# Optimization experiments

Measured on AMD Instinct MI355X. Metric: run time of the kernel, lower is better.

## Reference

```python
import jax, jax.numpy as jnp
import numpy as np

HEADS = 16
HEAD_DIM = 64  # embed_size // heads = 1024 // 16


def setup_inputs() -> dict:
    key = jax.random.key(0)
    ks = jax.random.split(key, 9)
    N, Sq, E, C = 4, 2048, 1024, 512
    Skv = 2 * Sq  # keys/values seq must equal doubled query seq (see view trick)
    return {
        "values": jax.random.normal(ks[0], (N, Skv, E), dtype=jnp.float32),
        "keys": jax.random.normal(ks[1], (N, Skv, E), dtype=jnp.float32),
        "queries": jax.random.normal(ks[2], (N, Sq, E), dtype=jnp.float32),
        "mask": jax.random.randint(ks[3], (N, Skv, HEADS, HEADS), 0, 2, dtype=jnp.int32),
        "condition": jax.random.normal(ks[4], (N, Sq, C), dtype=jnp.float32),
        "Wc": jax.random.normal(ks[5], (E, C), dtype=jnp.float32) * 0.02,
        "bc": jax.random.normal(ks[6], (E,), dtype=jnp.float32) * 0.02,
        "Wo": jax.random.normal(ks[7], (E, E), dtype=jnp.float32) * 0.02,
        "bo": jax.random.normal(ks[8], (E,), dtype=jnp.float32) * 0.02,
    }


def reference(values, keys, queries, mask, condition, Wc, bc, Wo, bo):
    N = queries.shape[0]
    H, D = HEADS, HEAD_DIM
    # condition_linear + concat: (N, Sq, 2E) -> view doubles seq -> (N, 2Sq, H, D)
    cond_feat = jnp.einsum('nsc,ec->nse', condition, Wc) + bc
    cq = jnp.concatenate([queries, cond_feat], axis=-1).reshape(N, -1, H, D)
    k = keys.reshape(N, -1, H, D)    # (N, 2Sq, H, D)
    v = values.reshape(N, -1, H, D)  # (N, 2Sq, H, D)
    # per-(batch,seq) heads-by-heads attention, exactly as the torch matmul does
    att = jnp.einsum('nshd,nsed->nshe', cq, k) / jnp.sqrt(jnp.float32(D))
    att = jnp.where(mask == 0, jnp.float32(-1e20), att)
    att = jax.nn.softmax(att, axis=-1)
    out = jnp.einsum('nshe,nsed->nshd', att, v).reshape(N, -1, H * D)
    return jnp.einsum('nsk,ek->nse', out, Wo) + bo
```

## Files before the change

kernel.cpp:

```cpp
#include <hip/hip_runtime.h>
#include <hip/hip_bf16.h>
#include <type_traits>

#define NB   4
#define SQ   2048
#define SKV  4096
#define EMB  1024
#define CDIM 512
#define POS  4

typedef __attribute__((ext_vector_type(8))) short short8;
typedef __attribute__((ext_vector_type(4))) float f32x4;

__device__ __forceinline__ float b2f(ushort u) {
    union { unsigned int i; float f; } v;
    v.i = ((unsigned int)u) << 16;
    return v.f;
}
__device__ __forceinline__ ushort f2b(float f) {
    union { float f; unsigned int i; } v; v.f = f;
    unsigned int x = v.i;
    return (ushort)((x + 0x7fffu + ((x >> 16) & 1u)) >> 16);
}

__device__ __forceinline__ void glds16(const ushort* gp, ushort* lp) {
    __builtin_amdgcn_global_load_lds(
        (const __attribute__((address_space(1))) unsigned int*)gp,
        (__attribute__((address_space(3))) unsigned int*)lp,
        16, 0, 0);
}

__global__ __launch_bounds__(256)
void cvt_f32_bf16(const float* __restrict__ in, ushort* __restrict__ out, int n4)
{
    const int i = blockIdx.x * 256 + threadIdx.x;
    if (i < n4) {
        float4 v = ((const float4*)in)[i];
        ushort4 o;
        o.x = f2b(v.x); o.y = f2b(v.y); o.z = f2b(v.z); o.w = f2b(v.w);
        ((ushort4*)out)[i] = o;
    }
}

template <typename OT>
__global__ __launch_bounds__(256)
void gemm_bt_bias(const ushort* __restrict__ A, const ushort* __restrict__ B,
                  const float* __restrict__ bias, OT* __restrict__ C,
                  int M, int Nn, int K)
{
    __shared__ __attribute__((aligned(16))) ushort As[128 * 32];
    __shared__ __attribute__((aligned(16))) ushort Bs[128 * 32];

    const int tid  = threadIdx.x;
    const int wave = tid >> 6;
    const int lane = tid & 63;
    const int quad = lane >> 4;
    const int l16  = lane & 15;
    const int wr   = wave >> 1;
    const int wc   = wave & 1;

    int mTile, nTile;
    {
        const int gx = gridDim.x, gy = gridDim.y;
        const int flat = blockIdx.y * gx + blockIdx.x;
        if ((gx & 7) == 0 && gy == 8) {
            const int c = flat & 7, j = flat >> 3;
            mTile = c * (gx >> 3) + (j >> 3);
            nTile = j & 7;
        } else {
            mTile = blockIdx.x; nTile = blockIdx.y;
        }
    }
    const long mBase = (long)mTile * 128;
    const long nBase = (long)nTile * 128;

    const ushort* Ablk = A + mBase * K;
    const ushort* Bblk = B + nBase * K;

    const int lr = lane >> 2;
    const int lc = (lane & 3) * 8;
    const int c0 = wave * 2, c1 = wave * 2 + 1;
    const ushort* aG0 = Ablk + (long)(c0 * 16 + lr) * K + lc;
    const ushort* aG1 = Ablk + (long)(c1 * 16 + lr) * K + lc;
    const ushort* bG0 = Bblk + (long)(c0 * 16 + lr) * K + lc;
    const ushort* bG1 = Bblk + (long)(c1 * 16 + lr) * K + lc;
    ushort* aL0 = As + c0 * 512;
    ushort* aL1 = As + c1 * 512;
    ushort* bL0 = Bs + c0 * 512;
    ushort* bL1 = Bs + c1 * 512;

    f32x4 acc[4][4];
#pragma unroll
    for (int i = 0; i < 4; ++i)
#pragma unroll
        for (int j = 0; j < 4; ++j)
            acc[i][j] = (f32x4){0.f, 0.f, 0.f, 0.f};

    for (int k0 = 0; k0 < K; k0 += 32) {
        __syncthreads();
        glds16(aG0 + k0, aL0);
        glds16(aG1 + k0, aL1);
        glds16(bG0 + k0, bL0);
        glds16(bG1 + k0, bL1);
        __syncthreads();

        short8 af[4], bfr[4];
#pragma unroll
        for (int mt = 0; mt < 4; ++mt)
            af[mt] = *(const short8*)(As + (wr * 64 + mt * 16 + l16) * 32 + quad * 8);
#pragma unroll
        for (int nt = 0; nt < 4; ++nt)
            bfr[nt] = *(const short8*)(Bs + (wc * 64 + nt * 16 + l16) * 32 + quad * 8);

#pragma unroll
        for (int mt = 0; mt < 4; ++mt)
#pragma unroll
            for (int nt = 0; nt < 4; ++nt)
                acc[mt][nt] = __builtin_amdgcn_mfma_f32_16x16x32_bf16(
                    af[mt], bfr[nt], acc[mt][nt], 0, 0, 0);
    }

#pragma unroll
    for (int mt = 0; mt < 4; ++mt) {
#pragma unroll
        for (int nt = 0; nt < 4; ++nt) {
            const long n = nBase + wc * 64 + nt * 16 + l16;
            const float bv = bias[n];
#pragma unroll
            for (int r = 0; r < 4; ++r) {
                const long m = mBase + wr * 64 + mt * 16 + quad * 4 + r;
                if constexpr (std::is_same<OT, float>::value)
                    C[m * Nn + n] = acc[mt][nt][r] + bv;
                else
                    C[m * Nn + n] = f2b(acc[mt][nt][r] + bv);
            }
        }
    }
}

__global__ __launch_bounds__(256)
void attn_kernel(const float*  __restrict__ queries,
                 const ushort* __restrict__ condfeat,
                 const float*  __restrict__ keys,
                 const float*  __restrict__ values,
                 const int*    __restrict__ mask,
                 ushort* __restrict__ attout)
{
    const int tid     = threadIdx.x;
    const int basePos = blockIdx.x * POS;

    __shared__ __attribute__((aligned(16))) float cq[16 * 68];
    __shared__ __attribute__((aligned(16))) float ks[16 * 68];
    __shared__ __attribute__((aligned(16))) float vs[16 * 68];
    __shared__ float sc[16 * 17];

    const int base4 = tid * 4;
    const int hs = base4 >> 6, dsd = base4 & 63;

    auto loadQ = [&](int p) -> float4 {
        const int n = p >> 12, sh = (p & 4095) >> 1;
        float4 q4;
        if (p & 1) {
            const ushort* cp = condfeat + ((size_t)n * SQ + sh) * EMB + base4;
            ushort4 c4 = *(const ushort4*)cp;
            q4.x = b2f(c4.x); q4.y = b2f(c4.y); q4.z = b2f(c4.z); q4.w = b2f(c4.w);
        } else {
            q4 = *(const float4*)(queries + ((size_t)n * SQ + sh) * EMB + base4);
        }
        return q4;
    };

    float4 q4 = loadQ(basePos);
    float4 k4 = *(const float4*)(keys   + ((size_t)basePos << 10) + base4);
    float4 v4 = *(const float4*)(values + ((size_t)basePos << 10) + base4);
    int    mv = mask[((size_t)basePos << 8) + tid];

#pragma unroll
    for (int i = 0; i < POS; ++i) {
        const int p = basePos + i;

        *(float4*)(cq + hs * 68 + dsd) = q4;
        *(float4*)(ks + hs * 68 + dsd) = k4;
        *(float4*)(vs + hs * 68 + dsd) = v4;
        __syncthreads();

        float4 q4n, k4n, v4n; int mvn = 0;
        if (i + 1 < POS) {
            q4n = loadQ(p + 1);
            k4n = *(const float4*)(keys   + ((size_t)(p + 1) << 10) + base4);
            v4n = *(const float4*)(values + ((size_t)(p + 1) << 10) + base4);
            mvn = mask[((size_t)(p + 1) << 8) + tid];
        }

        {
            const int h = tid >> 4, e = tid & 15;
            float s = 0.f;
#pragma unroll
            for (int d = 0; d < 64; d += 4) {
                float4 a = *(const float4*)(cq + h * 68 + d);
                float4 b = *(const float4*)(ks + e * 68 + d);
                s += a.x * b.x + a.y * b.y + a.z * b.z + a.w * b.w;
            }
            s *= 0.125f;
            s = (mv == 0) ? -1e20f : s;

            float mx = s;
#pragma unroll
            for (int d = 1; d < 16; d <<= 1)
                mx = fmaxf(mx, __shfl_xor(mx, d));
            const float ex = __expf(s - mx);
            float sum = ex;
#pragma unroll
            for (int d = 1; d < 16; d <<= 1)
                sum += __shfl_xor(sum, d);
            sc[h * 17 + e] = ex / sum;
        }
        __syncthreads();

        {
            float4 a = {0.f, 0.f, 0.f, 0.f};
#pragma unroll
            for (int e = 0; e < 16; ++e) {
                const float pe = sc[hs * 17 + e];
                float4 vv = *(const float4*)(vs + e * 68 + dsd);
                a.x += pe * vv.x; a.y += pe * vv.y;
                a.z += pe * vv.z; a.w += pe * vv.w;
            }
            ushort4 o;
            o.x = f2b(a.x); o.y = f2b(a.y); o.z = f2b(a.z); o.w = f2b(a.w);
            *(ushort4*)(attout + ((size_t)p << 10) + base4) = o;
        }

        if (i + 1 < POS) {
            __syncthreads();
            q4 = q4n; k4 = k4n; v4 = v4n; mv = mvn;
        }
    }
}

extern "C" void kernel_launch(void* const* d_in, const int* in_sizes, int n_in,
                              void* d_out, int out_size, void* d_ws, size_t ws_size,
                              hipStream_t stream)
{
    const float* values    = (const float*)d_in[0];
    const float* keys      = (const float*)d_in[1];
    const float* queries   = (const float*)d_in[2];
    const int*   mask      = (const int*)  d_in[3];
    const float* condition = (const float*)d_in[4];
    const float* Wc        = (const float*)d_in[5];
    const float* bc        = (const float*)d_in[6];
    const float* Wo        = (const float*)d_in[7];
    const float* bo        = (const float*)d_in[8];
    float* out = (float*)d_out;

    ushort* condfeat = (ushort*)d_ws;
    ushort* attout   = condfeat + (size_t)NB * SQ * EMB;
    ushort* cond_bf  = attout;
    ushort* Wc_bf    = attout + (size_t)NB * SQ * CDIM;
    ushort* Wo_bf    = condfeat;

    cvt_f32_bf16<<<(NB * SQ * CDIM / 4 + 255) / 256, 256, 0, stream>>>(
        condition, cond_bf, NB * SQ * CDIM / 4);
    cvt_f32_bf16<<<(EMB * CDIM / 4 + 255) / 256, 256, 0, stream>>>(
        Wc, Wc_bf, EMB * CDIM / 4);

    {
        dim3 grid((NB * SQ) / 128, EMB / 128);
        gemm_bt_bias<ushort><<<grid, 256, 0, stream>>>(
            cond_bf, Wc_bf, bc, condfeat, NB * SQ, EMB, CDIM);
    }

    attn_kernel<<<(NB * SKV) / POS, 256, 0, stream>>>(queries, condfeat, keys,
                                                      values, mask, attout);

    cvt_f32_bf16<<<(EMB * EMB / 4 + 255) / 256, 256, 0, stream>>>(
        Wo, Wo_bf, EMB * EMB / 4);

    {
        dim3 grid((NB * SKV) / 128, EMB / 128);
        gemm_bt_bias<float><<<grid, 256, 0, stream>>>(
            attout, Wo_bf, bo, out, NB * SKV, EMB, EMB);
    }
}
```

Measured before the change: 311.8 us.

## Rewrite per-position attention with one wave per position using bf16 MFMA

The attention kernel now gives each wave its own sequence position instead of looping four positions through the whole block with block-wide barriers. The 16x16 head score matrix and the probability-times-V product are computed with bf16 MFMA instructions, with K and Q converted to bf16 in registers. V is staged into shared memory through asynchronous global-to-LDS loads, and softmax uses a few lane shuffles. This removes __syncthreads and scalar LDS dot products, but adds bf16 rounding of K, Q, V and the probabilities, plus lane-shuffle packing of the probability operand.

```diff
diff --git a/kernel.cpp b/kernel.cpp
--- a/kernel.cpp
+++ b/kernel.cpp
@@ -7,7 +7,6 @@
 #define SKV  4096
 #define EMB  1024
 #define CDIM 512
-#define POS  4
 
 typedef __attribute__((ext_vector_type(8))) short short8;
 typedef __attribute__((ext_vector_type(4))) float f32x4;
@@ -146,95 +145,108 @@
                  const int*    __restrict__ mask,
                  ushort* __restrict__ attout)
 {
-    const int tid     = threadIdx.x;
-    const int basePos = blockIdx.x * POS;
-
-    __shared__ __attribute__((aligned(16))) float cq[16 * 68];
-    __shared__ __attribute__((aligned(16))) float ks[16 * 68];
-    __shared__ __attribute__((aligned(16))) float vs[16 * 68];
-    __shared__ float sc[16 * 17];
-
-    const int base4 = tid * 4;
-    const int hs = base4 >> 6, dsd = base4 & 63;
-
-    auto loadQ = [&](int p) -> float4 {
-        const int n = p >> 12, sh = (p & 4095) >> 1;
-        float4 q4;
-        if (p & 1) {
-            const ushort* cp = condfeat + ((size_t)n * SQ + sh) * EMB + base4;
-            ushort4 c4 = *(const ushort4*)cp;
-            q4.x = b2f(c4.x); q4.y = b2f(c4.y); q4.z = b2f(c4.z); q4.w = b2f(c4.w);
-        } else {
-            q4 = *(const float4*)(queries + ((size_t)n * SQ + sh) * EMB + base4);
-        }
-        return q4;
-    };
-
-    float4 q4 = loadQ(basePos);
-    float4 k4 = *(const float4*)(keys   + ((size_t)basePos << 10) + base4);
-    float4 v4 = *(const float4*)(values + ((size_t)basePos << 10) + base4);
-    int    mv = mask[((size_t)basePos << 8) + tid];
-
-#pragma unroll
-    for (int i = 0; i < POS; ++i) {
-        const int p = basePos + i;
-
-        *(float4*)(cq + hs * 68 + dsd) = q4;
-        *(float4*)(ks + hs * 68 + dsd) = k4;
-        *(float4*)(vs + hs * 68 + dsd) = v4;
-        __syncthreads();
-
-        float4 q4n, k4n, v4n; int mvn = 0;
-        if (i + 1 < POS) {
-            q4n = loadQ(p + 1);
-            k4n = *(const float4*)(keys   + ((size_t)(p + 1) << 10) + base4);
-            v4n = *(const float4*)(values + ((size_t)(p + 1) << 10) + base4);
-            mvn = mask[((size_t)(p + 1) << 8) + tid];
-        }
-
-        {
-            const int h = tid >> 4, e = tid & 15;
-            float s = 0.f;
-#pragma unroll
-            for (int d = 0; d < 64; d += 4) {
-                float4 a = *(const float4*)(cq + h * 68 + d);
-                float4 b = *(const float4*)(ks + e * 68 + d);
-                s += a.x * b.x + a.y * b.y + a.z * b.z + a.w * b.w;
-            }
-            s *= 0.125f;
-            s = (mv == 0) ? -1e20f : s;
-
-            float mx = s;
-#pragma unroll
-            for (int d = 1; d < 16; d <<= 1)
-                mx = fmaxf(mx, __shfl_xor(mx, d));
-            const float ex = __expf(s - mx);
-            float sum = ex;
-#pragma unroll
-            for (int d = 1; d < 16; d <<= 1)
-                sum += __shfl_xor(sum, d);
-            sc[h * 17 + e] = ex / sum;
-        }
-        __syncthreads();
-
-        {
-            float4 a = {0.f, 0.f, 0.f, 0.f};
-#pragma unroll
-            for (int e = 0; e < 16; ++e) {
-                const float pe = sc[hs * 17 + e];
-                float4 vv = *(const float4*)(vs + e * 68 + dsd);
-                a.x += pe * vv.x; a.y += pe * vv.y;
-                a.z += pe * vv.z; a.w += pe * vv.w;
-            }
-            ushort4 o;
-            o.x = f2b(a.x); o.y = f2b(a.y); o.z = f2b(a.z); o.w = f2b(a.w);
-            *(ushort4*)(attout + ((size_t)p << 10) + base4) = o;
-        }
-
-        if (i + 1 < POS) {
-            __syncthreads();
-            q4 = q4n; k4 = k4n; v4 = v4n; mv = mvn;
-        }
+    __shared__ __attribute__((aligned(16))) float vbuf[4][1024];
+
+    const int tid  = threadIdx.x;
+    const int wave = tid >> 6;
+    const int lane = tid & 63;
+    const int l15  = lane & 15;
+    const int quad = lane >> 4;
+    const int p    = blockIdx.x * 4 + wave;
+    const int n    = p >> 12;
+    const int sh   = (p & 4095) >> 1;
+
+    float* vb = vbuf[wave];
+    const float* vrow = values + ((size_t)p << 10);
+#pragma unroll
+    for (int c = 0; c < 4; ++c)
+        glds16((const ushort*)(vrow + c * 256 + lane * 4),
+               (ushort*)(vb + c * 256));
+
+    const int4 mv = *(const int4*)(mask + ((size_t)p << 8) + l15 * 16 + quad * 4);
+
+    union SU { short8 v; ushort u[8]; uint w[4]; };
+
+    const float* krow = keys + ((size_t)p << 10);
+    SU ka, kb;
+    {
+        float kf[16];
+        *(float4*)&kf[0]  = *(const float4*)(krow + l15 * 64 + quad * 8);
+        *(float4*)&kf[4]  = *(const float4*)(krow + l15 * 64 + quad * 8 + 4);
+        *(float4*)&kf[8]  = *(const float4*)(krow + l15 * 64 + 32 + quad * 8);
+        *(float4*)&kf[12] = *(const float4*)(krow + l15 * 64 + 32 + quad * 8 + 4);
+#pragma unroll
+        for (int j = 0; j < 8; ++j) { ka.u[j] = f2b(kf[j]); kb.u[j] = f2b(kf[8 + j]); }
+    }
+
+    SU qa, qb;
+    if (p & 1) {
+        const ushort* crow = condfeat + (((size_t)n * SQ + sh) << 10);
+        qa.v = *(const short8*)(crow + l15 * 64 + quad * 8);
+        qb.v = *(const short8*)(crow + l15 * 64 + 32 + quad * 8);
+    } else {
+        const float* qrow = queries + (((size_t)n * SQ + sh) << 10);
+        float qf[16];
+        *(float4*)&qf[0]  = *(const float4*)(qrow + l15 * 64 + quad * 8);
+        *(float4*)&qf[4]  = *(const float4*)(qrow + l15 * 64 + quad * 8 + 4);
+        *(float4*)&qf[8]  = *(const float4*)(qrow + l15 * 64 + 32 + quad * 8);
+        *(float4*)&qf[12] = *(const float4*)(qrow + l15 * 64 + 32 + quad * 8 + 4);
+#pragma unroll
+        for (int j = 0; j < 8; ++j) { qa.u[j] = f2b(qf[j]); qb.u[j] = f2b(qf[8 + j]); }
+    }
+
+    f32x4 sacc = (f32x4){0.f, 0.f, 0.f, 0.f};
+    sacc = __builtin_amdgcn_mfma_f32_16x16x32_bf16(ka.v, qa.v, sacc, 0, 0, 0);
+    sacc = __builtin_amdgcn_mfma_f32_16x16x32_bf16(kb.v, qb.v, sacc, 0, 0, 0);
+
+    float s0 = (mv.x == 0) ? -1e20f : sacc[0] * 0.125f;
+    float s1 = (mv.y == 0) ? -1e20f : sacc[1] * 0.125f;
+    float s2 = (mv.z == 0) ? -1e20f : sacc[2] * 0.125f;
+    float s3 = (mv.w == 0) ? -1e20f : sacc[3] * 0.125f;
+
+    float mx = fmaxf(fmaxf(s0, s1), fmaxf(s2, s3));
+    mx = fmaxf(mx, __shfl_xor(mx, 16));
+    mx = fmaxf(mx, __shfl_xor(mx, 32));
+    const float e0 = __expf(s0 - mx), e1 = __expf(s1 - mx);
+    const float e2 = __expf(s2 - mx), e3 = __expf(s3 - mx);
+    float sum = e0 + e1 + e2 + e3;
+    sum += __shfl_xor(sum, 16);
+    sum += __shfl_xor(sum, 32);
+    const float inv = 1.f / sum;
+
+    const uint pk01 = (uint)f2b(e0 * inv) | ((uint)f2b(e1 * inv) << 16);
+    const uint pk23 = (uint)f2b(e2 * inv) | ((uint)f2b(e3 * inv) << 16);
+
+    const int srcA = (quad * 32 + l15) & 63;
+    const int srcB = (quad * 32 + 16 + l15) & 63;
+    SU pf;
+    {
+        const uint w0 = (uint)__shfl((int)pk01, srcA);
+        const uint w1 = (uint)__shfl((int)pk23, srcA);
+        const uint w2 = (uint)__shfl((int)pk01, srcB);
+        const uint w3 = (uint)__shfl((int)pk23, srcB);
+        const bool lo = (lane < 32);
+        pf.w[0] = lo ? w0 : 0u; pf.w[1] = lo ? w1 : 0u;
+        pf.w[2] = lo ? w2 : 0u; pf.w[3] = lo ? w3 : 0u;
+    }
+
+    asm volatile("s_waitcnt vmcnt(0)" ::: "memory");
+
+    ushort* orow = attout + ((size_t)p << 10);
+    const int eb = (quad & 1) * 8;
+#pragma unroll
+    for (int sl = 0; sl < 4; ++sl) {
+        const int d0 = sl * 16;
+        SU vf;
+#pragma unroll
+        for (int j = 0; j < 8; ++j)
+            vf.u[j] = f2b(vb[(eb + j) * 64 + d0 + l15]);
+        f32x4 oacc = (f32x4){0.f, 0.f, 0.f, 0.f};
+        oacc = __builtin_amdgcn_mfma_f32_16x16x32_bf16(vf.v, pf.v, oacc, 0, 0, 0);
+        ushort4 o;
+        o.x = f2b(oacc[0]); o.y = f2b(oacc[1]);
+        o.z = f2b(oacc[2]); o.w = f2b(oacc[3]);
+        *(ushort4*)(orow + l15 * 64 + d0 + quad * 4) = o;
     }
 }
 
@@ -270,8 +282,8 @@
             cond_bf, Wc_bf, bc, condfeat, NB * SQ, EMB, CDIM);
     }
 
-    attn_kernel<<<(NB * SKV) / POS, 256, 0, stream>>>(queries, condfeat, keys,
-                                                      values, mask, attout);
+    attn_kernel<<<(NB * SKV) / 4, 256, 0, stream>>>(queries, condfeat, keys,
+                                                    values, mask, attout);
 
     cvt_f32_bf16<<<(EMB * EMB / 4 + 255) / 256, 256, 0, stream>>>(
         Wo, Wo_bf, EMB * EMB / 4);
```

New measurement: 301.6 us. 1.03x faster.
